# Performance work log

Measured on AMD Instinct MI355X. Metric: run time of the kernel, lower is better.

Reference implementation:

```python
import jax, jax.numpy as jnp
import numpy as np

NV, NE, NT = 20000, 40000, 30000
D, H, L = 512, 8, 2
HD = D // H
SCALE = float(np.sqrt(HD))
EV, EE, ET = 160000, 160000, 120000
LN_EPS = 1e-5


def _layer_norm(x, g, b):
    m = jnp.mean(x, axis=-1, keepdims=True)
    v = jnp.mean((x - m) ** 2, axis=-1, keepdims=True)
    return (x - m) * jax.lax.rsqrt(v + LN_EPS) * g + b


def _attn_layer(x, ei, W, b, g, bt):
    # x: [N, D]; ei: [2, E]; W: [4, D, D] (q,k,v,out); b: [4, D]
    n = x.shape[0]
    resid = x
    q = (x @ W[0] + b[0]).reshape(n, H, HD)
    k = (x @ W[1] + b[1]).reshape(n, H, HD)
    v = (x @ W[2] + b[2]).reshape(n, H, HD)
    src, dst = ei[0], ei[1]
    # per-edge scores: query at target, key at source (k[edge_index[1]] gather in original)
    scores = jnp.sum(q[dst] * k[src], axis=-1) / SCALE        # [E, H]
    # NOTE: original applies softmax over dim=0, i.e. globally over the edge axis
    w = jax.nn.softmax(scores, axis=0)                         # [E, H]
    msgs = w[:, :, None] * v[src]                              # [E, H, HD]
    out = jax.ops.segment_sum(msgs, dst, num_segments=n)      # [N, H, HD]
    out = out.reshape(n, D) @ W[3] + b[3]
    return _layer_norm(out + resid, g, bt)


def _attn_stack(x, ei, W, b, g, bt):
    for l in range(L):
        x = _attn_layer(x, ei, W[l], b[l], g[l], bt[l])
    return x


def setup_inputs() -> dict:
    key = jax.random.key(0)
    ks = jax.random.split(key, 16)
    inp = {}
    inp['vertices'] = jax.random.normal(ks[0], (NV, D), jnp.float32)
    inp['edge_features'] = jax.random.normal(ks[1], (NE, D), jnp.float32)
    inp['triangle_features'] = jax.random.normal(ks[2], (NT, D), jnp.float32)
    inp['v_embed'] = jax.random.normal(ks[3], (NV, D), jnp.float32)
    inp['e_embed'] = jax.random.normal(ks[4], (NE, D), jnp.float32)
    inp['t_embed'] = jax.random.normal(ks[5], (NT, D), jnp.float32)
    inp['v_pos'] = jax.random.normal(ks[6], (NV, D), jnp.float32) * 0.1
    inp['e_pos'] = jax.random.normal(ks[7], (NE, D), jnp.float32) * 0.1
    inp['t_pos'] = jax.random.normal(ks[8], (NT, D), jnp.float32) * 0.1
    for name, k2 in (('v', ks[9]), ('e', ks[10]), ('t', ks[11])):
        inp[name + 'W'] = jax.random.normal(k2, (L, 4, D, D), jnp.float32) * 0.02
        inp[name + 'B'] = jnp.zeros((L, 4, D), jnp.float32)
        inp[name + 'G'] = jnp.ones((L, D), jnp.float32)
        inp[name + 'Bt'] = jnp.zeros((L, D), jnp.float32)
    inp['head_W'] = jax.random.normal(ks[12], (3, D, D), jnp.float32) * 0.02
    inp['head_b'] = jnp.zeros((3, D), jnp.float32)
    inp['v_ei'] = jax.random.randint(ks[13], (2, EV), 0, NV, jnp.int32)
    inp['e_ei'] = jax.random.randint(ks[14], (2, EE), 0, NE, jnp.int32)
    inp['t_ei'] = jax.random.randint(ks[15], (2, ET), 0, NT, jnp.int32)
    return inp


def reference(vertices, edge_features, triangle_features, v_embed, e_embed, t_embed,
              v_pos, e_pos, t_pos, vW, vB, vG, vBt, eW, eB, eG, eBt,
              tW, tB, tG, tBt, head_W, head_b, v_ei, e_ei, t_ei):
    # embedding(arange(N)) == full table lookup; add positional params and input features
    v = v_embed + v_pos + vertices
    e = e_embed + e_pos + edge_features
    t = t_embed + t_pos + triangle_features
    v = _attn_stack(v, v_ei, vW, vB, vG, vBt)
    e = _attn_stack(e, e_ei, eW, eB, eG, eBt)
    t = _attn_stack(t, t_ei, tW, tB, tG, tBt)
    v_out = v @ head_W[0] + head_b[0]
    e_out = e @ head_W[1] + head_b[1]
    t_out = t @ head_W[2] + head_b[2]
    return (v_out, e_out, t_out)
```

## Files before the change

### kernel.cpp

```cpp
#include <hip/hip_runtime.h>


typedef __attribute__((ext_vector_type(8))) __bf16 bf16x8;
typedef __attribute__((ext_vector_type(4))) float f32x4;
typedef __attribute__((ext_vector_type(8))) unsigned short ushort8v;
typedef __attribute__((ext_vector_type(4))) unsigned short ushort4v;

__device__ __forceinline__ float b2f(unsigned short u) {
  union { unsigned u; float f; } x; x.u = (unsigned)u << 16; return x.f;
}
__device__ __forceinline__ unsigned short f2b(float f) {
  union { float f; unsigned u; } x; x.f = f;
  unsigned r = x.u + 0x7fffu + ((x.u >> 16) & 1u);
  return (unsigned short)(r >> 16);
}

__global__ __launch_bounds__(256) void init_x_kernel(
    const float4* __restrict__ a, const float4* __restrict__ b,
    const float4* __restrict__ c, unsigned short* __restrict__ xb,
    long long n4)
{
  long long stride = (long long)gridDim.x * 256;
  for (long long i = (long long)blockIdx.x * 256 + threadIdx.x; i < n4; i += stride) {
    float4 av = a[i], bv = b[i], cv = c[i];
    ushort4v o;
    o.x = f2b(av.x + bv.x + cv.x); o.y = f2b(av.y + bv.y + cv.y);
    o.z = f2b(av.z + bv.z + cv.z); o.w = f2b(av.w + bv.w + cv.w);
    *(ushort4v*)(xb + i * 4) = o;
  }
}

__global__ __launch_bounds__(256) void transpose_w_kernel(
    const float* __restrict__ W, unsigned short* __restrict__ WT)
{
  __shared__ float t[32][33];
  const float* src = W + (size_t)blockIdx.z * 262144;
  unsigned short* dst = WT + (size_t)blockIdx.z * 262144;
  int bx = blockIdx.x * 32, by = blockIdx.y * 32;
  int tx = threadIdx.x, ty = threadIdx.y;
  #pragma unroll
  for (int i = 0; i < 32; i += 8)
    t[ty + i][tx] = src[(size_t)(by + ty + i) * 512 + bx + tx];
  __syncthreads();
  #pragma unroll
  for (int i = 0; i < 32; i += 8) {
    int c = bx + ty + i;
    int p = (c & ~0x3C) | ((c & 0x30) >> 2) | ((c & 0x0C) << 2);
    dst[(size_t)p * 512 + by + tx] = f2b(t[tx][ty + i]);
  }
}

__device__ __forceinline__ void stage16(const void* g, void* lds_uniform) {
  __builtin_amdgcn_global_load_lds(
      (const __attribute__((address_space(1))) void*)g,
      (__attribute__((address_space(3))) void*)lds_uniform, 16, 0, 0);
}
__device__ __forceinline__ int xcd_swizzle(int orig, int nwg) {
  const int xcd = orig & 7, lin = orig >> 3;
  const int q = nwg >> 3, r8 = nwg & 7;
  return (xcd < r8 ? xcd * (q + 1) : r8 * (q + 1) + (xcd - r8) * q) + lin;
}

template<int OUT_BF16>
__global__ __launch_bounds__(512, 2) void gemm_bt_kernel(
    const unsigned short* __restrict__ A,
    const unsigned short* __restrict__ BT,
    const float* __restrict__ bias,
    void* __restrict__ Cv,
    int M, int Ncols)
{
  constexpr int K = 512;
  __shared__ unsigned short smem[65536];

  const int wgid = xcd_swizzle(blockIdx.x, gridDim.x);
  const int tiles_n = Ncols >> 8;
  const int tm = wgid / tiles_n;
  const int tn = wgid - tm * tiles_n;
  const int row0 = tm << 8, col0 = tn << 8;
  const int lane = threadIdx.x & 63, wid = threadIdx.x >> 6;
  const int wr = (wid >> 2) << 7;
  const int wc = (wid & 3) << 6;

  f32x4 acc[8][4];
  #pragma unroll
  for (int i = 0; i < 8; ++i)
    #pragma unroll
    for (int j = 0; j < 4; ++j) acc[i][j] = (f32x4)0.f;

  int srow[4], scsw[4], sseg[4];
  #pragma unroll
  for (int i = 0; i < 4; ++i) {
    int seg = (i << 3) | wid;
    int idx = (seg << 6) | lane;
    int row = idx >> 3, ch = idx & 7;
    sseg[i] = seg; srow[i] = row; scsw[i] = ch ^ (row & 7);
  }

  #define STG_PAIR(buf, kb_, i)                                               \
    { int ra = row0 + srow[i]; ra = (ra < M) ? ra : (M - 1);                  \
      stage16(A + (size_t)ra * K + (kb_) + (scsw[i] << 3),                    \
              smem + (buf) * 32768 + (sseg[i] << 9));                         \
      int rb = col0 + srow[i];                                                \
      stage16(BT + (size_t)rb * K + (kb_) + (scsw[i] << 3),                   \
              smem + (buf) * 32768 + 16384 + (sseg[i] << 9)); }

  STG_PAIR(0, 0, 0) STG_PAIR(0, 0, 1) STG_PAIR(0, 0, 2) STG_PAIR(0, 0, 3)
  __syncthreads();
// ... 57 lines not shown
      #pragma unroll
      for (int ni = 0; ni < 4; ++ni)
        acc[mi][ni] = __builtin_amdgcn_mfma_f32_16x16x32_bf16(
            bv[ni], av[mi], acc[mi][ni], 0, 0, 0);
    __builtin_amdgcn_s_setprio(0);
    __builtin_amdgcn_s_barrier();

    #pragma unroll
    for (int i = 0; i < 4; ++i) av[i] = rdA(4 + i, 1);
    __builtin_amdgcn_s_barrier();
    __builtin_amdgcn_s_setprio(1);
    #pragma unroll
    for (int mi = 0; mi < 4; ++mi)
      #pragma unroll
      for (int ni = 0; ni < 4; ++ni)
        acc[4 + mi][ni] = __builtin_amdgcn_mfma_f32_16x16x32_bf16(
            bv[ni], av[mi], acc[4 + mi][ni], 0, 0, 0);
    __builtin_amdgcn_s_setprio(0);

    __syncthreads();
  }
  #undef STG_PAIR

  const int mrow = lane & 15;
  const int t4 = (lane >> 4) << 4;
  float bsv[16];
  #pragma unroll
  for (int ni = 0; ni < 4; ++ni) {
    float4 bvv = *(const float4*)(bias + col0 + wc + t4 + (ni << 2));
    bsv[4*ni+0] = bvv.x; bsv[4*ni+1] = bvv.y; bsv[4*ni+2] = bvv.z; bsv[4*ni+3] = bvv.w;
  }

  if (OUT_BF16) {
    unsigned short* C = (unsigned short*)Cv;
    #pragma unroll
    for (int mi = 0; mi < 8; ++mi) {
      int rowg = row0 + wr + (mi << 4) + mrow;
      if (rowg < M) {
        ushort8v o0, o1;
        #pragma unroll
        for (int r = 0; r < 4; ++r) {
          o0[r]     = f2b(acc[mi][0][r] + bsv[r]);
          o0[4 + r] = f2b(acc[mi][1][r] + bsv[4 + r]);
          o1[r]     = f2b(acc[mi][2][r] + bsv[8 + r]);
          o1[4 + r] = f2b(acc[mi][3][r] + bsv[12 + r]);
        }
        unsigned short* cp = C + (size_t)rowg * Ncols + col0 + wc + t4;
        *(ushort8v*)cp = o0;
        *(ushort8v*)(cp + 8) = o1;
      }
    }
  } else {
    float* C = (float*)Cv;
    #pragma unroll
    for (int mi = 0; mi < 8; ++mi) {
      int rowg = row0 + wr + (mi << 4) + mrow;
      if (rowg < M) {
        float* cp = C + (size_t)rowg * Ncols + col0 + wc + t4;
        #pragma unroll
        for (int ni = 0; ni < 4; ++ni) {
          float4 v;
          v.x = acc[mi][ni][0] + bsv[4*ni+0];
          v.y = acc[mi][ni][1] + bsv[4*ni+1];
          v.z = acc[mi][ni][2] + bsv[4*ni+2];
          v.w = acc[mi][ni][3] + bsv[4*ni+3];
          *(float4*)(cp + (ni << 2)) = v;
        }
      }
    }
  }
}

template<int OUT_BF16>
__global__ __launch_bounds__(256) void gemm_sm_kernel(
    const unsigned short* __restrict__ A,
    const unsigned short* __restrict__ BT,
    const float* __restrict__ bias,
    void* __restrict__ Cv,
    int M, int Ncols)
{
  constexpr int K = 512;
  __shared__ unsigned short As[8192];
  __shared__ unsigned short Bs[8192];

  const int wgid = xcd_swizzle(blockIdx.x, gridDim.x);
  const int tiles_n = Ncols >> 7;
  const int tm = wgid / tiles_n;
  const int tn = wgid - tm * tiles_n;
  const int row0 = tm << 7, col0 = tn << 7;
  const int lane = threadIdx.x & 63, wid = threadIdx.x >> 6;
  const int wm = (wid >> 1) << 6, wn = (wid & 1) << 6;

  f32x4 acc[4][4];
  #pragma unroll
  for (int i = 0; i < 4; ++i)
    #pragma unroll
    for (int j = 0; j < 4; ++j) acc[i][j] = (f32x4)0.f;

  int srow[4], scsw[4], sseg[4];
  #pragma unroll
  for (int i = 0; i < 4; ++i) {
    int seg = (i << 2) | wid;
    int idx = (seg << 6) | lane;
    int row = idx >> 3, ch = idx & 7;
    sseg[i] = seg; srow[i] = row; scsw[i] = ch ^ (row & 7);
  }

  #pragma unroll
  for (int kt = 0; kt < 8; ++kt) {
    const int kbase = kt << 6;
    #pragma unroll
    for (int i = 0; i < 4; ++i) {
      int ra = row0 + srow[i]; ra = (ra < M) ? ra : (M - 1);
      stage16(A + (size_t)ra * K + kbase + (scsw[i] << 3), As + (sseg[i] << 9));
      int rb = col0 + srow[i];
      stage16(BT + (size_t)rb * K + kbase + (scsw[i] << 3), Bs + (sseg[i] << 9));
    }
    asm volatile("s_waitcnt vmcnt(0)" ::: "memory");
// ... 3 lines not shown
    for (int kk = 0; kk < 2; ++kk) {
      const int kb = (kk << 6) + ((lane >> 4) << 4);
      bf16x8 af[4], bfr[4];
      #pragma unroll
      for (int mi = 0; mi < 4; ++mi) {
        int r = wm + (mi << 4) + (lane & 15);
        af[mi] = *(const bf16x8*)((const char*)As + (r << 7) + (kb ^ ((r & 7) << 4)));
      }
      #pragma unroll
      for (int ni = 0; ni < 4; ++ni) {
        int r = wn + (ni << 4) + (lane & 15);
        bfr[ni] = *(const bf16x8*)((const char*)Bs + (r << 7) + (kb ^ ((r & 7) << 4)));
      }
      #pragma unroll
      for (int mi = 0; mi < 4; ++mi)
        #pragma unroll
        for (int ni = 0; ni < 4; ++ni)
          acc[mi][ni] = __builtin_amdgcn_mfma_f32_16x16x32_bf16(
              bfr[ni], af[mi], acc[mi][ni], 0, 0, 0);
    }
    __syncthreads();
  }

  const int mrow = lane & 15;
  const int t4 = (lane >> 4) << 4;
  float bsv[16];
  #pragma unroll
  for (int ni = 0; ni < 4; ++ni) {
    float4 bvv = *(const float4*)(bias + col0 + wn + t4 + (ni << 2));
    bsv[4*ni+0] = bvv.x; bsv[4*ni+1] = bvv.y; bsv[4*ni+2] = bvv.z; bsv[4*ni+3] = bvv.w;
  }

  if (OUT_BF16) {
    unsigned short* C = (unsigned short*)Cv;
    #pragma unroll
    for (int mi = 0; mi < 4; ++mi) {
      int rowg = row0 + wm + (mi << 4) + mrow;
      if (rowg < M) {
        ushort8v o0, o1;
        #pragma unroll
        for (int r = 0; r < 4; ++r) {
          o0[r]     = f2b(acc[mi][0][r] + bsv[r]);
          o0[4 + r] = f2b(acc[mi][1][r] + bsv[4 + r]);
          o1[r]     = f2b(acc[mi][2][r] + bsv[8 + r]);
          o1[4 + r] = f2b(acc[mi][3][r] + bsv[12 + r]);
        }
        unsigned short* cp = C + (size_t)rowg * Ncols + col0 + wn + t4;
        *(ushort8v*)cp = o0;
        *(ushort8v*)(cp + 8) = o1;
      }
    }
  } else {
    float* C = (float*)Cv;
    #pragma unroll
    for (int mi = 0; mi < 4; ++mi) {
      int rowg = row0 + wm + (mi << 4) + mrow;
      if (rowg < M) {
        float* cp = C + (size_t)rowg * Ncols + col0 + wn + t4;
        #pragma unroll
        for (int ni = 0; ni < 4; ++ni) {
          float4 v;
          v.x = acc[mi][ni][0] + bsv[4*ni+0];
          v.y = acc[mi][ni][1] + bsv[4*ni+1];
          v.z = acc[mi][ni][2] + bsv[4*ni+2];
          v.w = acc[mi][ni][3] + bsv[4*ni+3];
          *(float4*)(cp + (ni << 2)) = v;
        }
      }
    }
  }
}

__global__ __launch_bounds__(256) void csr_scores_kernel(
    const unsigned short* __restrict__ qkv, const int* __restrict__ srcs,
    const int* __restrict__ rowptr, int N, float* __restrict__ sc,
    float* __restrict__ partm, float* __restrict__ parts)
{
  int wid = threadIdx.x >> 6, lane = threadIdx.x & 63;
  int n = (blockIdx.x << 2) | wid;
  float mx = -1e30f, sm = 0.f;
  if (n < N) {
    int beg = rowptr[n], end = rowptr[n + 1];
    if (beg < end) {
      ushort8v qv = *(const ushort8v*)(qkv + (size_t)n * 1536 + (lane << 3));
      float qf[8];
      #pragma unroll
      for (int j = 0; j < 8; ++j) qf[j] = b2f(qv[j]);
      int i = beg;
      for (; i + 2 <= end; i += 2) {
        int s0 = srcs[i], s1 = srcs[i + 1];
        ushort8v k0 = *(const ushort8v*)(qkv + (size_t)s0 * 1536 + 512 + (lane << 3));
        ushort8v k1 = *(const ushort8v*)(qkv + (size_t)s1 * 1536 + 512 + (lane << 3));
        float p0 = 0.f, p1 = 0.f;
        #pragma unroll
        for (int j = 0; j < 8; ++j) { p0 += qf[j] * b2f(k0[j]); p1 += qf[j] * b2f(k1[j]); }
        p0 += __shfl_xor(p0, 1); p1 += __shfl_xor(p1, 1);
        p0 += __shfl_xor(p0, 2); p1 += __shfl_xor(p1, 2);
        p0 += __shfl_xor(p0, 4); p1 += __shfl_xor(p1, 4);
        p0 *= 0.125f; p1 *= 0.125f;
        float nm = fmaxf(mx, fmaxf(p0, p1));
        sm = sm * __expf(mx - nm) + __expf(p0 - nm) + __expf(p1 - nm);
        mx = nm;
        if (!(lane & 7)) {
          sc[(size_t)i * 8 + (lane >> 3)] = p0;
          sc[(size_t)(i + 1) * 8 + (lane >> 3)] = p1;
        }
      }
      if (i < end) {
        int s0 = srcs[i];
        ushort8v k0 = *(const ushort8v*)(qkv + (size_t)s0 * 1536 + 512 + (lane << 3));
        float p0 = 0.f;
        #pragma unroll
        for (int j = 0; j < 8; ++j) p0 += qf[j] * b2f(k0[j]);
        p0 += __shfl_xor(p0, 1);
        p0 += __shfl_xor(p0, 2);
        p0 += __shfl_xor(p0, 4);
        p0 *= 0.125f;
        float nm = fmaxf(mx, p0);
        sm = sm * __expf(mx - nm) + __expf(p0 - nm);
        mx = nm;
        if (!(lane & 7)) sc[(size_t)i * 8 + (lane >> 3)] = p0;
      }
    }
  }
  if (!(lane & 7)) {
    size_t slot = ((size_t)blockIdx.x << 2) | wid;
    partm[slot * 8 + (lane >> 3)] = mx;
    parts[slot * 8 + (lane >> 3)] = sm;
  }
}

__device__ __forceinline__ void pair_reduce_block(
    float (&m)[8], float (&s)[8], float* redm, float* reds)
{
  int lane = threadIdx.x & 63, wid = threadIdx.x >> 6;
  #pragma unroll
  for (int h = 0; h < 8; ++h)
    #pragma unroll
    for (int off = 1; off < 64; off <<= 1) {
      float om = __shfl_xor(m[h], off);
      float os = __shfl_xor(s[h], off);
      float M = fmaxf(m[h], om);
      s[h] = s[h] * __expf(m[h] - M) + os * __expf(om - M);
      m[h] = M;
    }
  if (lane == 0) {
    #pragma unroll
    for (int h = 0; h < 8; ++h) { redm[h * 4 + wid] = m[h]; reds[h * 4 + wid] = s[h]; }
  }
  __syncthreads();
  if (threadIdx.x == 0) {
    #pragma unroll
    for (int h = 0; h < 8; ++h) {
      float M = redm[h * 4], S = reds[h * 4];
      #pragma unroll
      for (int w = 1; w < 4; ++w) {
        float om = redm[h * 4 + w], os = reds[h * 4 + w];
        float nM = fmaxf(M, om);
        S = S * __expf(M - nM) + os * __expf(om - nM);
        M = nM;
      }
      m[h] = M; s[h] = S;
    }
  }
}

__global__ __launch_bounds__(256) void gms_part_kernel(
    const float* __restrict__ pm, const float* __restrict__ ps, int nslots,
    float* __restrict__ pm2, float* __restrict__ ps2)
{
  __shared__ float redm[32], reds[32];
  float m[8], s[8];
  #pragma unroll
  for (int h = 0; h < 8; ++h) { m[h] = -1e30f; s[h] = 0.f; }
  int stride = gridDim.x * 256;
  for (int i = blockIdx.x * 256 + threadIdx.x; i < nslots; i += stride) {
    #pragma unroll
    for (int h = 0; h < 8; ++h) {
      float mi = pm[(size_t)i * 8 + h], si = ps[(size_t)i * 8 + h];
      float M = fmaxf(m[h], mi);
      s[h] = s[h] * __expf(m[h] - M) + si * __expf(mi - M);
      m[h] = M;
    }
  }
  pair_reduce_block(m, s, redm, reds);
  if (threadIdx.x == 0) {
    #pragma unroll
    for (int h = 0; h < 8; ++h) { pm2[blockIdx.x * 8 + h] = m[h]; ps2[blockIdx.x * 8 + h] = s[h]; }
  }
}

__global__ __launch_bounds__(256) void gms_final_kernel(
    const float* __restrict__ pm2, const float* __restrict__ ps2,
    float* __restrict__ gmax, float* __restrict__ ginv)
{
  __shared__ float redm[32], reds[32];
  float m[8], s[8];
  #pragma unroll
  for (int h = 0; h < 8; ++h) {
    m[h] = pm2[threadIdx.x * 8 + h];
    s[h] = ps2[threadIdx.x * 8 + h];
  }
  pair_reduce_block(m, s, redm, reds);
  if (threadIdx.x == 0) {
    #pragma unroll
    for (int h = 0; h < 8; ++h) { gmax[h] = m[h]; ginv[h] = 1.0f / s[h]; }
  }
}

__global__ __launch_bounds__(256) void hist_kernel(
    const int* __restrict__ ei, int E, int* __restrict__ deg)
{
  int e = blockIdx.x * 256 + threadIdx.x;
  if (e < E) atomicAdd(&deg[ei[E + e]], 1);
}

__global__ __launch_bounds__(1024) void scan_part_kernel(
    const int* __restrict__ deg, int N, int* __restrict__ rowptr,
    int* __restrict__ bsums)
{
  __shared__ int wsum[16];
  int i = blockIdx.x * 1024 + threadIdx.x;
  int lane = threadIdx.x & 63, wid = threadIdx.x >> 6;
  int sv = (i < N) ? deg[i] : 0;
  #pragma unroll
  for (int off = 1; off < 64; off <<= 1) {
    int t = __shfl_up(sv, off);
    if (lane >= off) sv += t;
  }
  if (lane == 63) wsum[wid] = sv;
  __syncthreads();
  if (threadIdx.x < 16) {
    int ws = wsum[threadIdx.x];
    #pragma unroll
    for (int off = 1; off < 16; off <<= 1) {
      int t = __shfl_up(ws, off);
      if (threadIdx.x >= off) ws += t;
    }
    wsum[threadIdx.x] = ws;
  }
  __syncthreads();
  if (wid > 0) sv += wsum[wid - 1];
  if (i < N) rowptr[i + 1] = sv;
  if (threadIdx.x == 1023) bsums[blockIdx.x] = sv;
}

__global__ __launch_bounds__(64) void scan_bsums_kernel(int* bsums, int nb)
{
  int lane = threadIdx.x;
  int v = (lane < nb) ? bsums[lane] : 0;
  #pragma unroll
  for (int off = 1; off < 64; off <<= 1) {
    int t = __shfl_up(v, off);
    if (lane >= off) v += t;
  }
  int ex = __shfl_up(v, 1);
  if (lane == 0) ex = 0;
  if (lane < nb) bsums[lane] = ex;
}

__global__ __launch_bounds__(1024) void scan_add_kernel(
    int* __restrict__ rowptr, const int* __restrict__ bsums, int N)
{
  int i = blockIdx.x * 1024 + threadIdx.x;
  if (i == 0) rowptr[0] = 0;
  if (i < N && blockIdx.x > 0) rowptr[i + 1] += bsums[blockIdx.x];
}

__global__ __launch_bounds__(256) void scatter_kernel(
    const int* __restrict__ ei, int E, const int* __restrict__ rowptr,
    int* __restrict__ cur, int* __restrict__ srcs)
{
  int e = blockIdx.x * 256 + threadIdx.x;
  if (e < E) {
    int dst = ei[E + e];
    int pos = atomicAdd(&cur[dst], 1);
    srcs[rowptr[dst] + pos] = ei[e];
  }
}

__global__ __launch_bounds__(256) void aggregate_kernel(
    const unsigned short* __restrict__ qkv, const float* __restrict__ sc,
    const float* __restrict__ gmax, const float* __restrict__ ginv,
    const int* __restrict__ srcs, const int* __restrict__ rowptr,
    int N, unsigned short* __restrict__ agg)
{
  int wid = threadIdx.x >> 6, lane = threadIdx.x & 63;
  int n = (blockIdx.x << 2) | wid;
  if (n >= N) return;
  int beg = rowptr[n], end = rowptr[n + 1];
  int h = lane >> 3;
  float gm = gmax[h];
  float inv = ginv[h];
  float acc[8] = {0.f,0.f,0.f,0.f,0.f,0.f,0.f,0.f};
  int i = beg;
  for (; i + 4 <= end; i += 4) {
    int s0 = srcs[i], s1 = srcs[i + 1], s2 = srcs[i + 2], s3 = srcs[i + 3];
    float w0 = __expf(sc[(size_t)i * 8 + h] - gm) * inv;
    float w1 = __expf(sc[(size_t)(i + 1) * 8 + h] - gm) * inv;
    float w2 = __expf(sc[(size_t)(i + 2) * 8 + h] - gm) * inv;
    float w3 = __expf(sc[(size_t)(i + 3) * 8 + h] - gm) * inv;
    ushort8v v0 = *(const ushort8v*)(qkv + (size_t)s0 * 1536 + 1024 + (lane << 3));
    ushort8v v1 = *(const ushort8v*)(qkv + (size_t)s1 * 1536 + 1024 + (lane << 3));
    ushort8v v2 = *(const ushort8v*)(qkv + (size_t)s2 * 1536 + 1024 + (lane << 3));
    ushort8v v3 = *(const ushort8v*)(qkv + (size_t)s3 * 1536 + 1024 + (lane << 3));
    #pragma unroll
    for (int j = 0; j < 8; ++j)
      acc[j] += (w0 * b2f(v0[j]) + w1 * b2f(v1[j]))
              + (w2 * b2f(v2[j]) + w3 * b2f(v3[j]));
  }
  for (; i < end; ++i) {
    int s0 = srcs[i];
    float w0 = __expf(sc[(size_t)i * 8 + h] - gm) * inv;
    ushort8v v0 = *(const ushort8v*)(qkv + (size_t)s0 * 1536 + 1024 + (lane << 3));
    #pragma unroll
    for (int j = 0; j < 8; ++j) acc[j] += w0 * b2f(v0[j]);
  }
  ushort8v o;
  #pragma unroll
  for (int j = 0; j < 8; ++j) o[j] = f2b(acc[j]);
  *(ushort8v*)(agg + (size_t)n * 512 + (lane << 3)) = o;
}

__global__ __launch_bounds__(256) void ln_kernel(
    const unsigned short* __restrict__ proj, const float* __restrict__ g,
    const float* __restrict__ bt, unsigned short* __restrict__ xb, int N)
{
  int wid = threadIdx.x >> 6, lane = threadIdx.x & 63;
  int n = (blockIdx.x << 2) | wid;
  if (n >= N) return;
  size_t base = (size_t)n * 512 + (lane << 3);
  ushort8v pv = *(const ushort8v*)(proj + base);
  ushort8v xv = *(const ushort8v*)(xb + base);
  float y[8];
  #pragma unroll
  for (int j = 0; j < 8; ++j) y[j] = b2f(pv[j]) + b2f(xv[j]);
  float s = 0.f;
  #pragma unroll
  for (int j = 0; j < 8; ++j) s += y[j];
  #pragma unroll
  for (int off = 1; off < 64; off <<= 1) s += __shfl_xor(s, off);
  float mean = s * (1.f / 512.f);
  float vs = 0.f;
  #pragma unroll
  for (int j = 0; j < 8; ++j) { float d = y[j] - mean; vs += d * d; }
  #pragma unroll
  for (int off = 1; off < 64; off <<= 1) vs += __shfl_xor(vs, off);
  float rstd = rsqrtf(vs * (1.f / 512.f) + 1e-5f);
  int gi = lane << 3;
  ushort8v ob;
  #pragma unroll
  for (int j = 0; j < 8; ++j)
    ob[j] = f2b((y[j] - mean) * rstd * g[gi + j] + bt[gi + j]);
  *(ushort8v*)(xb + base) = ob;
}

extern "C" void kernel_launch(void* const* d_in, const int* in_sizes, int n_in,
                              void* d_out, int out_size, void* d_ws, size_t ws_size,
                              hipStream_t stream)
{
  (void)n_in; (void)out_size;
  const float* feat[3] = {(const float*)d_in[0], (const float*)d_in[1], (const float*)d_in[2]};
  const float* emb[3]  = {(const float*)d_in[3], (const float*)d_in[4], (const float*)d_in[5]};
  const float* pos[3]  = {(const float*)d_in[6], (const float*)d_in[7], (const float*)d_in[8]};
  const float* W[3]  = {(const float*)d_in[9],  (const float*)d_in[13], (const float*)d_in[17]};
  const float* Bb[3] = {(const float*)d_in[10], (const float*)d_in[14], (const float*)d_in[18]};
  const float* G[3]  = {(const float*)d_in[11], (const float*)d_in[15], (const float*)d_in[19]};
  const float* Bt[3] = {(const float*)d_in[12], (const float*)d_in[16], (const float*)d_in[20]};
  const float* headW = (const float*)d_in[21];
  const float* headB = (const float*)d_in[22];
  const int* ei[3] = {(const int*)d_in[23], (const int*)d_in[24], (const int*)d_in[25]};

  int Ns[3], Es[3];
  for (int s = 0; s < 3; ++s) { Ns[s] = in_sizes[s] / 512; Es[s] = in_sizes[23 + s] / 2; }
  int NMAX = Ns[0], EMAX = Es[0];
  for (int s = 1; s < 3; ++s) { if (Ns[s] > NMAX) NMAX = Ns[s]; if (Es[s] > EMAX) EMAX = Es[s]; }

  char* base = (char*)d_ws;
  size_t off = 0;
  auto carve = [&](size_t bytes) -> char* {
    char* r = base + off;
    off += (bytes + 255) & ~(size_t)255;
    return r;
  };
  unsigned short* WT  = (unsigned short*)carve((size_t)27 * 262144 * 2);
  unsigned short* XB  = (unsigned short*)carve((size_t)NMAX * 512 * 2);
  unsigned short* QKV = (unsigned short*)carve((size_t)NMAX * 1536 * 2);
  float*          SC  = (float*)carve((size_t)EMAX * 8 * 4);
  unsigned short* AGG = (unsigned short*)carve((size_t)NMAX * 512 * 2);
  int*   ROWPTR = (int*)carve((size_t)(NMAX + 1) * 4);
  int*   DEG    = (int*)carve((size_t)NMAX * 4);
  int*   SRCS   = (int*)carve((size_t)EMAX * 4);
  int*   BSUMS  = (int*)carve(64 * 4);
  float* PARTM  = (float*)carve((size_t)(NMAX + 8) * 8 * 4);
  float* PARTS1 = (float*)carve((size_t)(NMAX + 8) * 8 * 4);
  float* PARTM2 = (float*)carve(256 * 8 * 4);
  float* PARTS2 = (float*)carve(256 * 8 * 4);
  float* GMAX   = (float*)carve(256);
  float* GINV   = (float*)carve(256);
  unsigned short* PROJ = QKV;
  if (off > ws_size) return;

  transpose_w_kernel<<<dim3(16,16,8), dim3(32,8), 0, stream>>>(W[0], WT);
  transpose_w_kernel<<<dim3(16,16,8), dim3(32,8), 0, stream>>>(W[1], WT + (size_t)8 * 262144);
  transpose_w_kernel<<<dim3(16,16,8), dim3(32,8), 0, stream>>>(W[2], WT + (size_t)16 * 262144);
  transpose_w_kernel<<<dim3(16,16,3), dim3(32,8), 0, stream>>>(headW, WT + (size_t)24 * 262144);

  size_t out_off = 0;
  for (int s = 0; s < 3; ++s) {
    const int N = Ns[s], E = Es[s];
    const int mt = (N + 255) >> 8;
    const int mts = (N + 127) >> 7;
    const int nb = (N + 1023) / 1024;
    const int nsb = (N + 3) / 4;

    init_x_kernel<<<2048, 256, 0, stream>>>(
        (const float4*)feat[s], (const float4*)emb[s], (const float4*)pos[s],
        XB, (long long)N * 128);

    hipMemsetAsync(DEG, 0, (size_t)N * 4, stream);
    hist_kernel<<<(E + 255) / 256, 256, 0, stream>>>(ei[s], E, DEG);
    scan_part_kernel<<<nb, 1024, 0, stream>>>(DEG, N, ROWPTR, BSUMS);
    scan_bsums_kernel<<<1, 64, 0, stream>>>(BSUMS, nb);
    scan_add_kernel<<<nb, 1024, 0, stream>>>(ROWPTR, BSUMS, N);
    hipMemsetAsync(DEG, 0, (size_t)N * 4, stream);
    scatter_kernel<<<(E + 255) / 256, 256, 0, stream>>>(ei[s], E, ROWPTR, DEG, SRCS);

    for (int l = 0; l < 2; ++l) {
      const unsigned short* Wqkv = WT + (size_t)(s * 8 + l * 4) * 262144;
      const unsigned short* Wo   = WT + (size_t)(s * 8 + l * 4 + 3) * 262144;
      const float* bqkv = Bb[s] + (size_t)l * 4 * 512;
      const float* bo   = Bb[s] + (size_t)(l * 4 + 3) * 512;

      gemm_bt_kernel<1><<<dim3(mt * 6), 512, 0, stream>>>(XB, Wqkv, bqkv, QKV, N, 1536);
      csr_scores_kernel<<<nsb, 256, 0, stream>>>(QKV, SRCS, ROWPTR, N, SC, PARTM, PARTS1);
      gms_part_kernel<<<256, 256, 0, stream>>>(PARTM, PARTS1, nsb * 4, PARTM2, PARTS2);
      gms_final_kernel<<<1, 256, 0, stream>>>(PARTM2, PARTS2, GMAX, GINV);
      aggregate_kernel<<<nsb, 256, 0, stream>>>(QKV, SC, GMAX, GINV, SRCS, ROWPTR, N, AGG);
      gemm_sm_kernel<1><<<dim3(mts * 4), 256, 0, stream>>>(AGG, Wo, bo, PROJ, N, 512);
      ln_kernel<<<nsb, 256, 0, stream>>>(PROJ, G[s] + (size_t)l * 512,
                                         Bt[s] + (size_t)l * 512, XB, N);
    }

    gemm_sm_kernel<0><<<dim3(mts * 4), 256, 0, stream>>>(
        XB, WT + (size_t)(24 + s) * 262144, headB + (size_t)s * 512,
        (float*)d_out + out_off, N, 512);
    out_off += (size_t)N * 512;
  }
}
```

Before: 1.314 ms.

## Batch the three independent attention stacks into single grouped kernel launches

```diff
diff --git a/kernel.cpp b/kernel.cpp
--- a/kernel.cpp
+++ b/kernel.cpp
@@ -14,28 +14,81 @@
   unsigned r = x.u + 0x7fffu + ((x.u >> 16) & 1u);
   return (unsigned short)(r >> 16);
 }
-
-__global__ __launch_bounds__(256) void init_x_kernel(
-    const float4* __restrict__ a, const float4* __restrict__ b,
-    const float4* __restrict__ c, unsigned short* __restrict__ xb,
-    long long n4)
-{
+__device__ __forceinline__ int xcd_swizzle(int orig, int nwg) {
+  const int xcd = orig & 7, lin = orig >> 3;
+  const int q = nwg >> 3, r8 = nwg & 7;
+  return (xcd < r8 ? xcd * (q + 1) : r8 * (q + 1) + (xcd - r8) * q) + lin;
+}
+__device__ __forceinline__ void stage16(const void* g, void* lds_uniform) {
+  __builtin_amdgcn_global_load_lds(
+      (const __attribute__((address_space(1))) void*)g,
+      (__attribute__((address_space(3))) void*)lds_uniform, 16, 0, 0);
+}
+
+struct IB {
+  const float4* a[3]; const float4* b[3]; const float4* c[3];
+  unsigned short* xb[3];
+  long long cum[4];
+};
+struct HB {
+  const int* ei[3]; int E[3]; int cum[4];
+  int* deg[3]; const int* rowptr[3]; int* srcs[3];
+};
+struct PB {
+  const int* deg[3]; int* rowptr[3]; int N[3]; int nbcum[4];
+};
+struct GB {
+  const unsigned short* A[3]; const unsigned short* BT[3];
+  const float* bias[3]; void* C[3];
+  int M[3]; int cum[4];
+};
+struct SB {
+  const unsigned short* qkv[3]; const int* srcs[3]; const int* rowptr[3];
+  float* sc[3]; float* pm[3]; float* ps[3];
+  int N[3]; int cum[4];
+};
+struct MB {
+  const float* pm[3]; const float* ps[3]; int nslots[3];
+};
+struct AB {
+  const unsigned short* qkv[3]; const float* sc[3]; const int* srcs[3];
+  const int* rowptr[3]; unsigned short* agg[3];
+  int N[3]; int cum[4];
+};
+struct LB {
+  const unsigned short* proj[3]; const float* g[3]; const float* bt[3];
+  unsigned short* xb[3]; int N[3]; int cum[4];
+};
+__device__ __forceinline__ int find3(int b, const int* cum) {
+  return (b >= cum[1]) + (b >= cum[2]);
+}
+
+__global__ __launch_bounds__(256) void init_b_kernel(IB ib)
+{
+  long long total = ib.cum[3];
   long long stride = (long long)gridDim.x * 256;
-  for (long long i = (long long)blockIdx.x * 256 + threadIdx.x; i < n4; i += stride) {
-    float4 av = a[i], bv = b[i], cv = c[i];
+  for (long long i = (long long)blockIdx.x * 256 + threadIdx.x; i < total; i += stride) {
+    int s = (i >= ib.cum[1]) + (i >= ib.cum[2]);
+    long long j = i - ib.cum[s];
+    float4 av = ib.a[s][j], bv = ib.b[s][j], cv = ib.c[s][j];
     ushort4v o;
     o.x = f2b(av.x + bv.x + cv.x); o.y = f2b(av.y + bv.y + cv.y);
     o.z = f2b(av.z + bv.z + cv.z); o.w = f2b(av.w + bv.w + cv.w);
-    *(ushort4v*)(xb + i * 4) = o;
-  }
-}
-
-__global__ __launch_bounds__(256) void transpose_w_kernel(
-    const float* __restrict__ W, unsigned short* __restrict__ WT)
+    *(ushort4v*)(ib.xb[s] + j * 4) = o;
+  }
+}
+
+__global__ __launch_bounds__(256) void transpose_all_kernel(
+    const float* W0, const float* W1, const float* W2, const float* Wh,
+    unsigned short* WT)
 {
   __shared__ float t[32][33];
-  const float* src = W + (size_t)blockIdx.z * 262144;
-  unsigned short* dst = WT + (size_t)blockIdx.z * 262144;
+  int z = blockIdx.z;
+  const float* src = (z < 8)  ? W0 + (size_t)z * 262144
+                   : (z < 16) ? W1 + (size_t)(z - 8) * 262144
+                   : (z < 24) ? W2 + (size_t)(z - 16) * 262144
+                              : Wh + (size_t)(z - 24) * 262144;
+  unsigned short* dst = WT + (size_t)z * 262144;
   int bx = blockIdx.x * 32, by = blockIdx.y * 32;
   int tx = threadIdx.x, ty = threadIdx.y;
   #pragma unroll
@@ -50,29 +103,20 @@
   }
 }
 
-__device__ __forceinline__ void stage16(const void* g, void* lds_uniform) {
-  __builtin_amdgcn_global_load_lds(
-      (const __attribute__((address_space(1))) void*)g,
-      (__attribute__((address_space(3))) void*)lds_uniform, 16, 0, 0);
-}
-__device__ __forceinline__ int xcd_swizzle(int orig, int nwg) {
-  const int xcd = orig & 7, lin = orig >> 3;
-  const int q = nwg >> 3, r8 = nwg & 7;
-  return (xcd < r8 ? xcd * (q + 1) : r8 * (q + 1) + (xcd - r8) * q) + lin;
-}
-
 template<int OUT_BF16>
-__global__ __launch_bounds__(512, 2) void gemm_bt_kernel(
-    const unsigned short* __restrict__ A,
-    const unsigned short* __restrict__ BT,
-    const float* __restrict__ bias,
-    void* __restrict__ Cv,
-    int M, int Ncols)
+__global__ __launch_bounds__(512, 2) void gemm_big_kernel(GB gb, int Ncols)
 {
   constexpr int K = 512;
   __shared__ unsigned short smem[65536];
 
-  const int wgid = xcd_swizzle(blockIdx.x, gridDim.x);
+  const int b = blockIdx.x;
+  const int s = find3(b, gb.cum);
+  const int wgid = xcd_swizzle(b - gb.cum[s], gb.cum[s + 1] - gb.cum[s]);
+  const unsigned short* A  = gb.A[s];
+  const unsigned short* BT = gb.BT[s];
+  const float* bias = gb.bias[s];
+  const int M = gb.M[s];
+
   const int tiles_n = Ncols >> 8;
   const int tm = wgid / tiles_n;
   const int tn = wgid - tm * tiles_n;
@@ -196,7 +240,7 @@
   }
 
   if (OUT_BF16) {
-    unsigned short* C = (unsigned short*)Cv;
+    unsigned short* C = (unsigned short*)gb.C[s];
     #pragma unroll
     for (int mi = 0; mi < 8; ++mi) {
       int rowg = row0 + wr + (mi << 4) + mrow;
@@ -215,7 +259,7 @@
       }
     }
   } else {
-    float* C = (float*)Cv;
+    float* C = (float*)gb.C[s];
     #pragma unroll
     for (int mi = 0; mi < 8; ++mi) {
       int rowg = row0 + wr + (mi << 4) + mrow;
@@ -236,18 +280,20 @@
 }
 
 template<int OUT_BF16>
-__global__ __launch_bounds__(256) void gemm_sm_kernel(
-    const unsigned short* __restrict__ A,
-    const unsigned short* __restrict__ BT,
-    const float* __restrict__ bias,
-    void* __restrict__ Cv,
-    int M, int Ncols)
+__global__ __launch_bounds__(256) void gemm_sm_kernel(GB gb, int Ncols)
 {
   constexpr int K = 512;
   __shared__ unsigned short As[8192];
   __shared__ unsigned short Bs[8192];
 
-  const int wgid = xcd_swizzle(blockIdx.x, gridDim.x);
+  const int b = blockIdx.x;
+  const int s = find3(b, gb.cum);
+  const int wgid = xcd_swizzle(b - gb.cum[s], gb.cum[s + 1] - gb.cum[s]);
+  const unsigned short* A  = gb.A[s];
+  const unsigned short* BT = gb.BT[s];
+  const float* bias = gb.bias[s];
+  const int M = gb.M[s];
+
   const int tiles_n = Ncols >> 7;
   const int tm = wgid / tiles_n;
   const int tn = wgid - tm * tiles_n;
@@ -317,7 +363,7 @@
   }
 
   if (OUT_BF16) {
-    unsigned short* C = (unsigned short*)Cv;
+    unsigned short* C = (unsigned short*)gb.C[s];
     #pragma unroll
     for (int mi = 0; mi < 4; ++mi) {
       int rowg = row0 + wm + (mi << 4) + mrow;
@@ -336,7 +382,7 @@
       }
     }
   } else {
-    float* C = (float*)Cv;
+    float* C = (float*)gb.C[s];
     #pragma unroll
     for (int mi = 0; mi < 4; ++mi) {
       int rowg = row0 + wm + (mi << 4) + mrow;
@@ -356,16 +402,19 @@
   }
 }
 
-__global__ __launch_bounds__(256) void csr_scores_kernel(
-    const unsigned short* __restrict__ qkv, const int* __restrict__ srcs,
-    const int* __restrict__ rowptr, int N, float* __restrict__ sc,
-    float* __restrict__ partm, float* __restrict__ parts)
-{
+__global__ __launch_bounds__(256) void scores_b_kernel(SB sb)
+{
+  int b = blockIdx.x;
+  int s = find3(b, sb.cum);
+  int lb = b - sb.cum[s];
+  const unsigned short* qkv = sb.qkv[s];
+  const int* srcs = sb.srcs[s];
+  float* sc = sb.sc[s];
   int wid = threadIdx.x >> 6, lane = threadIdx.x & 63;
-  int n = (blockIdx.x << 2) | wid;
+  int n = (lb << 2) | wid;
   float mx = -1e30f, sm = 0.f;
-  if (n < N) {
-    int beg = rowptr[n], end = rowptr[n + 1];
+  if (n < sb.N[s]) {
+    int beg = sb.rowptr[s][n], end = sb.rowptr[s][n + 1];
     if (beg < end) {
       ushort8v qv = *(const ushort8v*)(qkv + (size_t)n * 1536 + (lane << 3));
       float qf[8];
@@ -409,9 +458,9 @@
     }
   }
   if (!(lane & 7)) {
-    size_t slot = ((size_t)blockIdx.x << 2) | wid;
-    partm[slot * 8 + (lane >> 3)] = mx;
-    parts[slot * 8 + (lane >> 3)] = sm;
+    size_t slot = ((size_t)lb << 2) | wid;
+    sb.pm[s][slot * 8 + (lane >> 3)] = mx;
+    sb.ps[s][slot * 8 + (lane >> 3)] = sm;
   }
 }
 
@@ -450,64 +499,70 @@
   }
 }
 
-__global__ __launch_bounds__(256) void gms_part_kernel(
-    const float* __restrict__ pm, const float* __restrict__ ps, int nslots,
-    float* __restrict__ pm2, float* __restrict__ ps2)
+__global__ __launch_bounds__(256) void gms_part_b_kernel(
+    MB mb, float* pm2, float* ps2)
 {
   __shared__ float redm[32], reds[32];
-  float m[8], s[8];
-  #pragma unroll
-  for (int h = 0; h < 8; ++h) { m[h] = -1e30f; s[h] = 0.f; }
-  int stride = gridDim.x * 256;
-  for (int i = blockIdx.x * 256 + threadIdx.x; i < nslots; i += stride) {
+  int s = blockIdx.x >> 8, j = blockIdx.x & 255;
+  const float* pm = mb.pm[s];
+  const float* ps = mb.ps[s];
+  float m[8], sv[8];
+  #pragma unroll
+  for (int h = 0; h < 8; ++h) { m[h] = -1e30f; sv[h] = 0.f; }
+  for (int i = j * 256 + threadIdx.x; i < mb.nslots[s]; i += 65536) {
     #pragma unroll
     for (int h = 0; h < 8; ++h) {
       float mi = pm[(size_t)i * 8 + h], si = ps[(size_t)i * 8 + h];
       float M = fmaxf(m[h], mi);
-      s[h] = s[h] * __expf(m[h] - M) + si * __expf(mi - M);
+      sv[h] = sv[h] * __expf(m[h] - M) + si * __expf(mi - M);
       m[h] = M;
     }
   }
-  pair_reduce_block(m, s, redm, reds);
+  pair_reduce_block(m, sv, redm, reds);
   if (threadIdx.x == 0) {
     #pragma unroll
-    for (int h = 0; h < 8; ++h) { pm2[blockIdx.x * 8 + h] = m[h]; ps2[blockIdx.x * 8 + h] = s[h]; }
-  }
-}
-
-__global__ __launch_bounds__(256) void gms_final_kernel(
-    const float* __restrict__ pm2, const float* __restrict__ ps2,
-    float* __restrict__ gmax, float* __restrict__ ginv)
+    for (int h = 0; h < 8; ++h) {
+      pm2[(s * 256 + j) * 8 + h] = m[h];
+      ps2[(s * 256 + j) * 8 + h] = sv[h];
+    }
+  }
+}
+
+__global__ __launch_bounds__(256) void gms_final_b_kernel(
+    const float* pm2, const float* ps2, float* gmax, float* ginv)
 {
   __shared__ float redm[32], reds[32];
-  float m[8], s[8];
+  int s = blockIdx.x;
+  float m[8], sv[8];
   #pragma unroll
   for (int h = 0; h < 8; ++h) {
-    m[h] = pm2[threadIdx.x * 8 + h];
-    s[h] = ps2[threadIdx.x * 8 + h];
-  }
-  pair_reduce_block(m, s, redm, reds);
+    m[h]  = pm2[(s * 256 + threadIdx.x) * 8 + h];
+    sv[h] = ps2[(s * 256 + threadIdx.x) * 8 + h];
+  }
+  pair_reduce_block(m, sv, redm, reds);
   if (threadIdx.x == 0) {
     #pragma unroll
-    for (int h = 0; h < 8; ++h) { gmax[h] = m[h]; ginv[h] = 1.0f / s[h]; }
-  }
-}
-
-__global__ __launch_bounds__(256) void hist_kernel(
-    const int* __restrict__ ei, int E, int* __restrict__ deg)
-{
-  int e = blockIdx.x * 256 + threadIdx.x;
-  if (e < E) atomicAdd(&deg[ei[E + e]], 1);
-}
-
-__global__ __launch_bounds__(1024) void scan_part_kernel(
-    const int* __restrict__ deg, int N, int* __restrict__ rowptr,
-    int* __restrict__ bsums)
+    for (int h = 0; h < 8; ++h) { gmax[s * 8 + h] = m[h]; ginv[s * 8 + h] = 1.0f / sv[h]; }
+  }
+}
+
+__global__ __launch_bounds__(256) void hist_b_kernel(HB hb)
+{
+  int b = blockIdx.x;
+  int s = find3(b, hb.cum);
+  int e = (b - hb.cum[s]) * 256 + threadIdx.x;
+  if (e < hb.E[s]) atomicAdd(&hb.deg[s][hb.ei[s][hb.E[s] + e]], 1);
+}
+
+__global__ __launch_bounds__(1024) void scan_part_b_kernel(PB pb, int* bsums)
 {
   __shared__ int wsum[16];
-  int i = blockIdx.x * 1024 + threadIdx.x;
+  int b = blockIdx.x;
+  int s = (b >= pb.nbcum[1]) + (b >= pb.nbcum[2]);
+  int lb = b - pb.nbcum[s];
+  int i = lb * 1024 + threadIdx.x;
   int lane = threadIdx.x & 63, wid = threadIdx.x >> 6;
-  int sv = (i < N) ? deg[i] : 0;
+  int sv = (i < pb.N[s]) ? pb.deg[s][i] : 0;
   #pragma unroll
   for (int off = 1; off < 64; off <<= 1) {
     int t = __shfl_up(sv, off);
@@ -526,14 +581,18 @@
   }
   __syncthreads();
   if (wid > 0) sv += wsum[wid - 1];
-  if (i < N) rowptr[i + 1] = sv;
-  if (threadIdx.x == 1023) bsums[blockIdx.x] = sv;
-}
-
-__global__ __launch_bounds__(64) void scan_bsums_kernel(int* bsums, int nb)
-{
+  if (i < pb.N[s]) pb.rowptr[s][i + 1] = sv;
+  if (threadIdx.x == 1023) bsums[s * 64 + lb] = sv;
+}
+
+__global__ __launch_bounds__(64) void scan_bsums_b_kernel(
+    int* bsums, int nb0, int nb1, int nb2)
+{
+  int s = blockIdx.x;
+  int nb = (s == 0) ? nb0 : (s == 1) ? nb1 : nb2;
+  int* bs = bsums + s * 64;
   int lane = threadIdx.x;
-  int v = (lane < nb) ? bsums[lane] : 0;
+  int v = (lane < nb) ? bs[lane] : 0;
   #pragma unroll
   for (int off = 1; off < 64; off <<= 1) {
     int t = __shfl_up(v, off);
@@ -541,42 +600,49 @@
   }
   int ex = __shfl_up(v, 1);
   if (lane == 0) ex = 0;
-  if (lane < nb) bsums[lane] = ex;
-}
-
-__global__ __launch_bounds__(1024) void scan_add_kernel(
-    int* __restrict__ rowptr, const int* __restrict__ bsums, int N)
-{
-  int i = blockIdx.x * 1024 + threadIdx.x;
-  if (i == 0) rowptr[0] = 0;
-  if (i < N && blockIdx.x > 0) rowptr[i + 1] += bsums[blockIdx.x];
-}
-
-__global__ __launch_bounds__(256) void scatter_kernel(
-    const int* __restrict__ ei, int E, const int* __restrict__ rowptr,
-    int* __restrict__ cur, int* __restrict__ srcs)
-{
-  int e = blockIdx.x * 256 + threadIdx.x;
-  if (e < E) {
-    int dst = ei[E + e];
-    int pos = atomicAdd(&cur[dst], 1);
-    srcs[rowptr[dst] + pos] = ei[e];
-  }
-}
-
-__global__ __launch_bounds__(256) void aggregate_kernel(
-    const unsigned short* __restrict__ qkv, const float* __restrict__ sc,
-    const float* __restrict__ gmax, const float* __restrict__ ginv,
-    const int* __restrict__ srcs, const int* __restrict__ rowptr,
-    int N, unsigned short* __restrict__ agg)
-{
+  if (lane < nb) bs[lane] = ex;
+}
+
+__global__ __launch_bounds__(1024) void scan_add_b_kernel(
+    PB pb, const int* bsums)
+{
+  int b = blockIdx.x;
+  int s = (b >= pb.nbcum[1]) + (b >= pb.nbcum[2]);
+  int lb = b - pb.nbcum[s];
+  int i = lb * 1024 + threadIdx.x;
+  if (lb == 0 && threadIdx.x == 0) pb.rowptr[s][0] = 0;
+  if (i < pb.N[s] && lb > 0) pb.rowptr[s][i + 1] += bsums[s * 64 + lb];
+}
+
+__global__ __launch_bounds__(256) void scatter_b_kernel(HB hb)
+{
+  int b = blockIdx.x;
+  int s = find3(b, hb.cum);
+  int e = (b - hb.cum[s]) * 256 + threadIdx.x;
+  if (e < hb.E[s]) {
+    const int* ei = hb.ei[s];
+    int dst = ei[hb.E[s] + e];
+    int pos = atomicAdd(&hb.deg[s][dst], 1);
+    hb.srcs[s][hb.rowptr[s][dst] + pos] = ei[e];
+  }
+}
+
+__global__ __launch_bounds__(256) void aggregate_b_kernel(
+    AB ab, const float* gmaxg, const float* ginvg)
+{
+  int b = blockIdx.x;
+  int s = find3(b, ab.cum);
+  int lb = b - ab.cum[s];
   int wid = threadIdx.x >> 6, lane = threadIdx.x & 63;
-  int n = (blockIdx.x << 2) | wid;
-  if (n >= N) return;
-  int beg = rowptr[n], end = rowptr[n + 1];
+  int n = (lb << 2) | wid;
+  if (n >= ab.N[s]) return;
+  const unsigned short* qkv = ab.qkv[s];
+  const float* sc = ab.sc[s];
+  const int* srcs = ab.srcs[s];
+  int beg = ab.rowptr[s][n], end = ab.rowptr[s][n + 1];
   int h = lane >> 3;
-  float gm = gmax[h];
-  float inv = ginv[h];
+  float gm  = gmaxg[s * 8 + h];
+  float inv = ginvg[s * 8 + h];
   float acc[8] = {0.f,0.f,0.f,0.f,0.f,0.f,0.f,0.f};
   int i = beg;
   for (; i + 4 <= end; i += 4) {
@@ -604,28 +670,29 @@
   ushort8v o;
   #pragma unroll
   for (int j = 0; j < 8; ++j) o[j] = f2b(acc[j]);
-  *(ushort8v*)(agg + (size_t)n * 512 + (lane << 3)) = o;
-}
-
-__global__ __launch_bounds__(256) void ln_kernel(
-    const unsigned short* __restrict__ proj, const float* __restrict__ g,
-    const float* __restrict__ bt, unsigned short* __restrict__ xb, int N)
-{
+  *(ushort8v*)(ab.agg[s] + (size_t)n * 512 + (lane << 3)) = o;
+}
+
+__global__ __launch_bounds__(256) void ln_b_kernel(LB lb_)
+{
+  int b = blockIdx.x;
+  int s = find3(b, lb_.cum);
+  int lb = b - lb_.cum[s];
   int wid = threadIdx.x >> 6, lane = threadIdx.x & 63;
-  int n = (blockIdx.x << 2) | wid;
-  if (n >= N) return;
+  int n = (lb << 2) | wid;
+  if (n >= lb_.N[s]) return;
   size_t base = (size_t)n * 512 + (lane << 3);
-  ushort8v pv = *(const ushort8v*)(proj + base);
-  ushort8v xv = *(const ushort8v*)(xb + base);
+  ushort8v pv = *(const ushort8v*)(lb_.proj[s] + base);
+  ushort8v xv = *(const ushort8v*)(lb_.xb[s] + base);
   float y[8];
   #pragma unroll
   for (int j = 0; j < 8; ++j) y[j] = b2f(pv[j]) + b2f(xv[j]);
-  float s = 0.f;
-  #pragma unroll
-  for (int j = 0; j < 8; ++j) s += y[j];
-  #pragma unroll
-  for (int off = 1; off < 64; off <<= 1) s += __shfl_xor(s, off);
-  float mean = s * (1.f / 512.f);
+  float sum = 0.f;
+  #pragma unroll
+  for (int j = 0; j < 8; ++j) sum += y[j];
+  #pragma unroll
+  for (int off = 1; off < 64; off <<= 1) sum += __shfl_xor(sum, off);
+  float mean = sum * (1.f / 512.f);
   float vs = 0.f;
   #pragma unroll
   for (int j = 0; j < 8; ++j) { float d = y[j] - mean; vs += d * d; }
@@ -636,8 +703,8 @@
   ushort8v ob;
   #pragma unroll
   for (int j = 0; j < 8; ++j)
-    ob[j] = f2b((y[j] - mean) * rstd * g[gi + j] + bt[gi + j]);
-  *(ushort8v*)(xb + base) = ob;
+    ob[j] = f2b((y[j] - mean) * rstd * lb_.g[s][gi + j] + lb_.bt[s][gi + j]);
+  *(ushort8v*)(lb_.xb[s] + base) = ob;
 }
 
 extern "C" void kernel_launch(void* const* d_in, const int* in_sizes, int n_in,
@@ -658,8 +725,14 @@
 
   int Ns[3], Es[3];
   for (int s = 0; s < 3; ++s) { Ns[s] = in_sizes[s] / 512; Es[s] = in_sizes[23 + s] / 2; }
-  int NMAX = Ns[0], EMAX = Es[0];
-  for (int s = 1; s < 3; ++s) { if (Ns[s] > NMAX) NMAX = Ns[s]; if (Es[s] > EMAX) EMAX = Es[s]; }
+
+  long long Noff[4] = {0}, Eoff[4] = {0}, Roff[4] = {0}, Poff[4] = {0};
+  for (int s = 0; s < 3; ++s) {
+    Noff[s + 1] = Noff[s] + Ns[s];
+    Eoff[s + 1] = Eoff[s] + Es[s];
+    Roff[s + 1] = Roff[s] + Ns[s] + 1;
+    Poff[s + 1] = Poff[s] + ((Ns[s] + 3) / 4) * 4;
+  }
 
   char* base = (char*)d_ws;
   size_t off = 0;
@@ -668,68 +741,152 @@
     off += (bytes + 255) & ~(size_t)255;
     return r;
   };
-  unsigned short* WT  = (unsigned short*)carve((size_t)27 * 262144 * 2);
-  unsigned short* XB  = (unsigned short*)carve((size_t)NMAX * 512 * 2);
-  unsigned short* QKV = (unsigned short*)carve((size_t)NMAX * 1536 * 2);
-  float*          SC  = (float*)carve((size_t)EMAX * 8 * 4);
-  unsigned short* AGG = (unsigned short*)carve((size_t)NMAX * 512 * 2);
-  int*   ROWPTR = (int*)carve((size_t)(NMAX + 1) * 4);
-  int*   DEG    = (int*)carve((size_t)NMAX * 4);
-  int*   SRCS   = (int*)carve((size_t)EMAX * 4);
-  int*   BSUMS  = (int*)carve(64 * 4);
-  float* PARTM  = (float*)carve((size_t)(NMAX + 8) * 8 * 4);
-  float* PARTS1 = (float*)carve((size_t)(NMAX + 8) * 8 * 4);
-  float* PARTM2 = (float*)carve(256 * 8 * 4);
-  float* PARTS2 = (float*)carve(256 * 8 * 4);
+  unsigned short* WT   = (unsigned short*)carve((size_t)27 * 262144 * 2);
+  unsigned short* XB   = (unsigned short*)carve((size_t)Noff[3] * 512 * 2);
+  unsigned short* QKV  = (unsigned short*)carve((size_t)Noff[3] * 1536 * 2);
+  float*          SC   = (float*)carve((size_t)Eoff[3] * 8 * 4);
+  unsigned short* AGG  = (unsigned short*)carve((size_t)Noff[3] * 512 * 2);
+  int*   ROWPTR = (int*)carve((size_t)Roff[3] * 4);
+  int*   DEG    = (int*)carve((size_t)Noff[3] * 4);
+  int*   SRCS   = (int*)carve((size_t)Eoff[3] * 4);
+  int*   BSUMS  = (int*)carve(3 * 64 * 4);
+  float* PARTM  = (float*)carve((size_t)Poff[3] * 8 * 4);
+  float* PARTS1 = (float*)carve((size_t)Poff[3] * 8 * 4);
+  float* PARTM2 = (float*)carve(3 * 256 * 8 * 4);
+  float* PARTS2 = (float*)carve(3 * 256 * 8 * 4);
   float* GMAX   = (float*)carve(256);
   float* GINV   = (float*)carve(256);
-  unsigned short* PROJ = QKV;
   if (off > ws_size) return;
 
-  transpose_w_kernel<<<dim3(16,16,8), dim3(32,8), 0, stream>>>(W[0], WT);
-  transpose_w_kernel<<<dim3(16,16,8), dim3(32,8), 0, stream>>>(W[1], WT + (size_t)8 * 262144);
-  transpose_w_kernel<<<dim3(16,16,8), dim3(32,8), 0, stream>>>(W[2], WT + (size_t)16 * 262144);
-  transpose_w_kernel<<<dim3(16,16,3), dim3(32,8), 0, stream>>>(headW, WT + (size_t)24 * 262144);
-
+  unsigned short* XBs[3];  unsigned short* QKVs[3]; float* SCs[3];
+  unsigned short* AGGs[3]; int* ROWPTRs[3]; int* DEGs[3]; int* SRCSs[3];
+  float* PMs[3]; float* PSs[3];
+  for (int s = 0; s < 3; ++s) {
+    XBs[s]  = XB  + Noff[s] * 512;
+    QKVs[s] = QKV + Noff[s] * 1536;
+    SCs[s]  = SC  + Eoff[s] * 8;
+    AGGs[s] = AGG + Noff[s] * 512;
+    ROWPTRs[s] = ROWPTR + Roff[s];
+    DEGs[s] = DEG + Noff[s];
+    SRCSs[s] = SRCS + Eoff[s];
+    PMs[s] = PARTM + Poff[s] * 8;
+    PSs[s] = PARTS1 + Poff[s] * 8;
+  }
+
+  transpose_all_kernel<<<dim3(16, 16, 27), dim3(32, 8), 0, stream>>>(
+      W[0], W[1], W[2], headW, WT);
+
+  IB ib;
+  for (int s = 0; s < 3; ++s) {
+    ib.a[s] = (const float4*)feat[s]; ib.b[s] = (const float4*)emb[s];
+    ib.c[s] = (const float4*)pos[s];  ib.xb[s] = XBs[s];
+  }
+  ib.cum[0] = 0;
+  for (int s = 0; s < 3; ++s) ib.cum[s + 1] = ib.cum[s] + (long long)Ns[s] * 128;
+  init_b_kernel<<<2048, 256, 0, stream>>>(ib);
+
+  HB hb;
+  hb.cum[0] = 0;
+  for (int s = 0; s < 3; ++s) {
+    hb.ei[s] = ei[s]; hb.E[s] = Es[s];
+    hb.cum[s + 1] = hb.cum[s] + (Es[s] + 255) / 256;
+    hb.deg[s] = DEGs[s]; hb.rowptr[s] = ROWPTRs[s]; hb.srcs[s] = SRCSs[s];
+  }
+  PB pb;
+  pb.nbcum[0] = 0;
+  for (int s = 0; s < 3; ++s) {
+    pb.deg[s] = DEGs[s]; pb.rowptr[s] = ROWPTRs[s]; pb.N[s] = Ns[s];
+    pb.nbcum[s + 1] = pb.nbcum[s] + (Ns[s] + 1023) / 1024;
+  }
+  hipMemsetAsync(DEG, 0, (size_t)Noff[3] * 4, stream);
+  hist_b_kernel<<<hb.cum[3], 256, 0, stream>>>(hb);
+  scan_part_b_kernel<<<pb.nbcum[3], 1024, 0, stream>>>(pb, BSUMS);
+  scan_bsums_b_kernel<<<3, 64, 0, stream>>>(
+      BSUMS, (Ns[0] + 1023) / 1024, (Ns[1] + 1023) / 1024, (Ns[2] + 1023) / 1024);
+  scan_add_b_kernel<<<pb.nbcum[3], 1024, 0, stream>>>(pb, BSUMS);
+  hipMemsetAsync(DEG, 0, (size_t)Noff[3] * 4, stream);
+  scatter_b_kernel<<<hb.cum[3], 256, 0, stream>>>(hb);
+
+  int nsbcum[4] = {0}, mtcum[4] = {0}, mtscum[4] = {0};
+  for (int s = 0; s < 3; ++s) {
+    nsbcum[s + 1] = nsbcum[s] + (Ns[s] + 3) / 4;
+    mtcum[s + 1]  = mtcum[s]  + ((Ns[s] + 255) >> 8) * 6;
+    mtscum[s + 1] = mtscum[s] + ((Ns[s] + 127) >> 7) * 4;
+  }
+
+  MB mb;
+  for (int s = 0; s < 3; ++s) {
+    mb.pm[s] = PMs[s]; mb.ps[s] = PSs[s];
+    mb.nslots[s] = ((Ns[s] + 3) / 4) * 4;
+  }
+
+  for (int l = 0; l < 2; ++l) {
+    GB qg;
+    for (int s = 0; s < 3; ++s) {
+      qg.A[s] = XBs[s];
+      qg.BT[s] = WT + (size_t)(s * 8 + l * 4) * 262144;
+      qg.bias[s] = Bb[s] + (size_t)l * 2048;
+      qg.C[s] = QKVs[s];
+      qg.M[s] = Ns[s];
+      qg.cum[s] = mtcum[s];
+    }
+    qg.cum[3] = mtcum[3];
+    gemm_big_kernel<1><<<mtcum[3], 512, 0, stream>>>(qg, 1536);
+
+    SB sb;
+    for (int s = 0; s < 3; ++s) {
+      sb.qkv[s] = QKVs[s]; sb.srcs[s] = SRCSs[s]; sb.rowptr[s] = ROWPTRs[s];
+      sb.sc[s] = SCs[s]; sb.pm[s] = PMs[s]; sb.ps[s] = PSs[s];
+      sb.N[s] = Ns[s]; sb.cum[s] = nsbcum[s];
+    }
+    sb.cum[3] = nsbcum[3];
+    scores_b_kernel<<<nsbcum[3], 256, 0, stream>>>(sb);
+
+    gms_part_b_kernel<<<768, 256, 0, stream>>>(mb, PARTM2, PARTS2);
+    gms_final_b_kernel<<<3, 256, 0, stream>>>(PARTM2, PARTS2, GMAX, GINV);
+
+    AB ab;
+    for (int s = 0; s < 3; ++s) {
+      ab.qkv[s] = QKVs[s]; ab.sc[s] = SCs[s]; ab.srcs[s] = SRCSs[s];
+      ab.rowptr[s] = ROWPTRs[s]; ab.agg[s] = AGGs[s];
+      ab.N[s] = Ns[s]; ab.cum[s] = nsbcum[s];
+    }
+    ab.cum[3] = nsbcum[3];
+    aggregate_b_kernel<<<nsbcum[3], 256, 0, stream>>>(ab, GMAX, GINV);
+
+    GB pg;
+    for (int s = 0; s < 3; ++s) {
+      pg.A[s] = AGGs[s];
+      pg.BT[s] = WT + (size_t)(s * 8 + l * 4 + 3) * 262144;
+      pg.bias[s] = Bb[s] + (size_t)(l * 2048 + 1536);
+      pg.C[s] = QKVs[s];
+      pg.M[s] = Ns[s];
+      pg.cum[s] = mtscum[s];
+    }
+    pg.cum[3] = mtscum[3];
+    gemm_sm_kernel<1><<<mtscum[3], 256, 0, stream>>>(pg, 512);
+
+    LB lb;
+    for (int s = 0; s < 3; ++s) {
+      lb.proj[s] = QKVs[s]; lb.g[s] = G[s] + (size_t)l * 512;
+      lb.bt[s] = Bt[s] + (size_t)l * 512; lb.xb[s] = XBs[s];
+      lb.N[s] = Ns[s]; lb.cum[s] = nsbcum[s];
+    }
+    lb.cum[3] = nsbcum[3];
+    ln_b_kernel<<<nsbcum[3], 256, 0, stream>>>(lb);
+  }
+
+  GB hg;
   size_t out_off = 0;
   for (int s = 0; s < 3; ++s) {
-    const int N = Ns[s], E = Es[s];
-    const int mt = (N + 255) >> 8;
-    const int mts = (N + 127) >> 7;
-    const int nb = (N + 1023) / 1024;
-    const int nsb = (N + 3) / 4;
-
-    init_x_kernel<<<2048, 256, 0, stream>>>(
-        (const float4*)feat[s], (const float4*)emb[s], (const float4*)pos[s],
-        XB, (long long)N * 128);
-
-    hipMemsetAsync(DEG, 0, (size_t)N * 4, stream);
-    hist_kernel<<<(E + 255) / 256, 256, 0, stream>>>(ei[s], E, DEG);
-    scan_part_kernel<<<nb, 1024, 0, stream>>>(DEG, N, ROWPTR, BSUMS);
-    scan_bsums_kernel<<<1, 64, 0, stream>>>(BSUMS, nb);
-    scan_add_kernel<<<nb, 1024, 0, stream>>>(ROWPTR, BSUMS, N);
-    hipMemsetAsync(DEG, 0, (size_t)N * 4, stream);
-    scatter_kernel<<<(E + 255) / 256, 256, 0, stream>>>(ei[s], E, ROWPTR, DEG, SRCS);
-
-    for (int l = 0; l < 2; ++l) {
-      const unsigned short* Wqkv = WT + (size_t)(s * 8 + l * 4) * 262144;
-      const unsigned short* Wo   = WT + (size_t)(s * 8 + l * 4 + 3) * 262144;
-      const float* bqkv = Bb[s] + (size_t)l * 4 * 512;
-      const float* bo   = Bb[s] + (size_t)(l * 4 + 3) * 512;
-
-      gemm_bt_kernel<1><<<dim3(mt * 6), 512, 0, stream>>>(XB, Wqkv, bqkv, QKV, N, 1536);
-      csr_scores_kernel<<<nsb, 256, 0, stream>>>(QKV, SRCS, ROWPTR, N, SC, PARTM, PARTS1);
-      gms_part_kernel<<<256, 256, 0, stream>>>(PARTM, PARTS1, nsb * 4, PARTM2, PARTS2);
-      gms_final_kernel<<<1, 256, 0, stream>>>(PARTM2, PARTS2, GMAX, GINV);
-      aggregate_kernel<<<nsb, 256, 0, stream>>>(QKV, SC, GMAX, GINV, SRCS, ROWPTR, N, AGG);
-      gemm_sm_kernel<1><<<dim3(mts * 4), 256, 0, stream>>>(AGG, Wo, bo, PROJ, N, 512);
-      ln_kernel<<<nsb, 256, 0, stream>>>(PROJ, G[s] + (size_t)l * 512,
-                                         Bt[s] + (size_t)l * 512, XB, N);
-    }
-
-    gemm_sm_kernel<0><<<dim3(mts * 4), 256, 0, stream>>>(
-        XB, WT + (size_t)(24 + s) * 262144, headB + (size_t)s * 512,
-        (float*)d_out + out_off, N, 512);
-    out_off += (size_t)N * 512;
-  }
-}
+    hg.A[s] = XBs[s];
+    hg.BT[s] = WT + (size_t)(24 + s) * 262144;
+    hg.bias[s] = headB + (size_t)s * 512;
+    hg.C[s] = (float*)d_out + out_off;
+    hg.M[s] = Ns[s];
+    hg.cum[s] = mtscum[s];
+    out_off += (size_t)Ns[s] * 512;
+  }
+  hg.cum[3] = mtscum[3];
+  gemm_sm_kernel<0><<<mtscum[3], 256, 0, stream>>>(hg, 512);
+}
```

Measured after the change: 1.220 ms. 1.08x faster.
